# Performance work log

Hardware: AMD Instinct MI355X
Metric: run time of the kernel (lower is better)

The kernel has to match this reference:

```python
import jax, jax.numpy as jnp
import numpy as np

# Default bone connections from BoneLengthLoss.__init__
BONES = np.array([(1, 2), (1, 3), (1, 4), (2, 5), (3, 6), (11, 12), (11, 13), (12, 14),
                  (13, 14), (14, 15), (15, 16), (16, 17), (12, 18), (18, 20), (20, 22),
                  (13, 19), (19, 21), (21, 23), (16, 24), (16, 25), (24, 26), (25, 26),
                  (24, 27), (27, 29), (29, 31), (25, 28), (28, 30), (30, 32), (17, 33),
                  (33, 34), (34, 35), (35, 36)], dtype=np.int32)
J1 = jnp.asarray(BONES[:, 0])
J2 = jnp.asarray(BONES[:, 1])

BATCH = 524288
NUM_KPTS = 37


def setup_inputs() -> dict:
    key = jax.random.key(0)
    k1, k2, k3 = jax.random.split(key, 3)
    pose_3d_pred = jax.random.normal(k1, (BATCH, NUM_KPTS, 3), dtype=jnp.float32)
    pose_3d_ref = jax.random.normal(k2, (BATCH, NUM_KPTS, 3), dtype=jnp.float32)
    valid_mask = jax.random.randint(k3, (BATCH, NUM_KPTS), 0, 2).astype(jnp.bool_)
    return {"pose_3d_pred": pose_3d_pred, "pose_3d_ref": pose_3d_ref,
            "valid_mask": valid_mask}


def reference(pose_3d_pred, pose_3d_ref, valid_mask):
    # Gather both endpoints of every bone: (B, n_bones, 3)
    pred_vec = pose_3d_pred[:, J2, :] - pose_3d_pred[:, J1, :]
    ref_vec = pose_3d_ref[:, J2, :] - pose_3d_ref[:, J1, :]
    pred_len = jnp.linalg.norm(pred_vec, axis=-1)  # (B, n_bones)
    ref_len = jnp.linalg.norm(ref_vec, axis=-1)    # (B, n_bones)
    # Bone is valid iff both endpoints are valid
    bone_valid = (valid_mask[:, J1] & valid_mask[:, J2]).astype(pred_len.dtype)
    # MSE over all valid (batch, bone) entries == mean over concatenated valid lengths
    sq_err = (pred_len - ref_len) ** 2
    num = jnp.sum(sq_err * bone_valid)
    den = jnp.sum(bone_valid)
    return num / den
```

## Files before the change

### kernel.cpp

```cpp
#include <hip/hip_runtime.h>


#define NKPT   37
#define ROWF   111
#define TROWS  32
#define TF4    888
#define WF4    222
#define TMW    296
#define WMW    74
#define TMI    1184
#define WMI    296
#define BLOCK  256
#define WPB    4
#define GRID   1280

__constant__ unsigned char c_j1[32] = {1,1,1,2,3,11,11,12,13,14,15,16,12,18,20,13,19,21,16,16,24,25,24,27,29,25,28,30,17,33,34,35};
__constant__ unsigned char c_j2[32] = {2,3,4,5,6,12,13,14,14,15,16,17,18,20,22,19,21,23,24,25,26,26,27,29,31,28,30,32,33,34,35,36};

__device__ __forceinline__ void glds16(const void* g, void* l) {
    __builtin_amdgcn_global_load_lds(
        (const __attribute__((address_space(1))) void*)g,
        (__attribute__((address_space(3))) void*)l, 16, 0, 0);
}
__device__ __forceinline__ void glds4(const void* g, void* l) {
    __builtin_amdgcn_global_load_lds(
        (const __attribute__((address_space(1))) void*)g,
        (__attribute__((address_space(3))) void*)l, 4, 0, 0);
}

__global__ void init_detect(const unsigned int* __restrict__ mw,
                            unsigned int* __restrict__ ws) {
    const int tid = threadIdx.x;
    if (tid < 4) ws[tid] = 0u;
    __syncthreads();
    unsigned int local = 0;
    for (int i = tid; i < 1024; i += BLOCK) local |= mw[i] & 0xFFFFFF00u;
    if (__any(local != 0) && (tid & 63) == 0) atomicOr(&ws[2], 1u);
}

template <bool MASK_BYTES>
__device__ __forceinline__ void tile_loop(
    const float4* __restrict__ pred4, const float4* __restrict__ ref4,
    const void* __restrict__ mask, int ntiles,
    float4* s_pose, unsigned char* s_mask,
    int wave, int lane, int row, const int* j1v, const int* j2v,
    float& num, unsigned int& den)
{
    unsigned int* s_mask_w = (unsigned int*)s_mask;
    const unsigned int* __restrict__ mw = (const unsigned int*)mask;
    const int* __restrict__ mi = (const int*)mask;
    const int sb = wave * WF4;

    for (int t = blockIdx.x; t < ntiles; t += GRID) {
        const float4* pb = pred4 + (size_t)t * TF4;
        const float4* rb = ref4  + (size_t)t * TF4;

        glds16(pb + sb + lane,       &s_pose[sb]);
        glds16(pb + sb + 64 + lane,  &s_pose[sb + 64]);
        glds16(pb + sb + 128 + lane, &s_pose[sb + 128]);
        glds16(rb + sb + lane,       &s_pose[TF4 + sb]);
        glds16(rb + sb + 64 + lane,  &s_pose[TF4 + sb + 64]);
        glds16(rb + sb + 128 + lane, &s_pose[TF4 + sb + 128]);
        if (lane < WF4 - 192) {
            glds16(pb + sb + 192 + lane, &s_pose[sb + 192]);
            glds16(rb + sb + 192 + lane, &s_pose[TF4 + sb + 192]);
        }
        if (MASK_BYTES) {
            const unsigned int* mb = mw + (size_t)t * TMW + wave * WMW;
            glds4(mb + lane, &s_mask_w[wave * WMW]);
            if (lane < WMW - 64)
                glds4(mb + 64 + lane, &s_mask_w[wave * WMW + 64]);
        } else {
            const int* mb = mi + (size_t)t * TMI + wave * WMI;
#pragma unroll
            for (int j = 0; j < 5; ++j) {
                int i = lane + 64 * j;
                if (i < WMI) s_mask[wave * WMI + i] = (unsigned char)mb[i];
            }
        }
        __syncthreads();

        const float* sp = (const float*)s_pose + row * ROWF;
        const float* sr = (const float*)(s_pose + TF4) + row * ROWF;
        const unsigned char* sm = s_mask + row * NKPT;
#pragma unroll
        for (int k = 0; k < 4; ++k) {
            const int a3 = j1v[k] * 3, b3 = j2v[k] * 3;
            float dx = sp[b3] - sp[a3];
            float dy = sp[b3 + 1] - sp[a3 + 1];
            float dz = sp[b3 + 2] - sp[a3 + 2];
            float pl = sqrtf(dx * dx + dy * dy + dz * dz);
            float ex = sr[b3] - sr[a3];
            float ey = sr[b3 + 1] - sr[a3 + 1];
            float ez = sr[b3 + 2] - sr[a3 + 2];
            float rl = sqrtf(ex * ex + ey * ey + ez * ez);
            unsigned int v = (unsigned int)(sm[j1v[k]] & sm[j2v[k]]);
            float d = pl - rl;
            num += v ? d * d : 0.0f;
            den += v;
        }
        __syncthreads();
    }
}

__global__ __launch_bounds__(BLOCK, 4)
void bone_main(const float* __restrict__ pred, const float* __restrict__ ref,
               const void* __restrict__ mask, int B,
               unsigned int* __restrict__ ws, float* __restrict__ out) {
    __shared__ __align__(16) float4 s_pose[2 * TF4];
    __shared__ __align__(4) unsigned char s_mask[TMI];
    __shared__ float s_rn[WPB];
    __shared__ unsigned int s_rd[WPB];

    const int tid  = threadIdx.x;
    const int wave = tid >> 6;
    const int lane = tid & 63;
    const int row  = tid & 31;
    const int grp  = (tid >> 5) & 7;

    int j1v[4], j2v[4];
#pragma unroll
    for (int k = 0; k < 4; ++k) {
        j1v[k] = (int)c_j1[grp * 4 + k];
        j2v[k] = (int)c_j2[grp * 4 + k];
    }

    const bool mask_bytes = (ws[2] != 0);
    const int ntiles = B / TROWS;

    float num = 0.0f;
    unsigned int den = 0u;

    if (mask_bytes)
        tile_loop<true>((const float4*)pred, (const float4*)ref, mask, ntiles,
                        s_pose, s_mask, wave, lane, row, j1v, j2v, num, den);
    else
        tile_loop<false>((const float4*)pred, (const float4*)ref, mask, ntiles,
                         s_pose, s_mask, wave, lane, row, j1v, j2v, num, den);

#pragma unroll
    for (int off = 32; off > 0; off >>= 1) {
        num += __shfl_down(num, off, 64);
        den += __shfl_down(den, off, 64);
    }
    if (lane == 0) { s_rn[wave] = num; s_rd[wave] = den; }
    __syncthreads();
    if (tid == 0) {
        float n = s_rn[0] + s_rn[1] + s_rn[2] + s_rn[3];
        unsigned int d = s_rd[0] + s_rd[1] + s_rd[2] + s_rd[3];
        atomicAdd((float*)&ws[0], n);
        atomicAdd(&ws[1], d);
        __threadfence();
        unsigned int prev = atomicAdd(&ws[3], 1u);
        if (prev == (unsigned int)(gridDim.x - 1)) {
            float fn = atomicAdd((float*)&ws[0], 0.0f);
            unsigned int fd = atomicAdd(&ws[1], 0u);
            out[0] = fn / (float)fd;
        }
    }
}

extern "C" void kernel_launch(void* const* d_in, const int* in_sizes, int n_in,
                              void* d_out, int out_size, void* d_ws, size_t ws_size,
                              hipStream_t stream) {
    const float* pred = (const float*)d_in[0];
    const float* ref  = (const float*)d_in[1];
    const void*  mask = d_in[2];
    const int n_mask  = in_sizes[2];
    const int B       = n_mask / NKPT;
    unsigned int* ws  = (unsigned int*)d_ws;

    init_detect<<<1, BLOCK, 0, stream>>>((const unsigned int*)mask, ws);
    bone_main<<<GRID, BLOCK, 0, stream>>>(pred, ref, mask, B, ws, (float*)d_out);
}
```

Before: 547.0 us.

## Double tile rows, share one LDS buffer for pred then ref, compile-time bones

Result: no change. 543.0 us (-0.7%).

```diff
diff --git a/kernel.cpp b/kernel.cpp
--- a/kernel.cpp
+++ b/kernel.cpp
@@ -3,19 +3,18 @@
 
 #define NKPT   37
 #define ROWF   111
-#define TROWS  32
-#define TF4    888
-#define WF4    222
-#define TMW    296
-#define WMW    74
-#define TMI    1184
-#define WMI    296
+#define TROWS  64
+#define TF4    1776
+#define WF4    444
+#define TMB    2368
+#define TMW    592
+#define WMW    148
 #define BLOCK  256
 #define WPB    4
 #define GRID   1280
 
-__constant__ unsigned char c_j1[32] = {1,1,1,2,3,11,11,12,13,14,15,16,12,18,20,13,19,21,16,16,24,25,24,27,29,25,28,30,17,33,34,35};
-__constant__ unsigned char c_j2[32] = {2,3,4,5,6,12,13,14,14,15,16,17,18,20,22,19,21,23,24,25,26,26,27,29,31,28,30,32,33,34,35,36};
+constexpr int J1[32] = {1,1,1,2,3,11,11,12,13,14,15,16,12,18,20,13,19,21,16,16,24,25,24,27,29,25,28,30,17,33,34,35};
+constexpr int J2[32] = {2,3,4,5,6,12,13,14,14,15,16,17,18,20,22,19,21,23,24,25,26,26,27,29,31,28,30,32,33,34,35,36};
 
 __device__ __forceinline__ void glds16(const void* g, void* l) {
     __builtin_amdgcn_global_load_lds(
@@ -38,105 +37,121 @@
     if (__any(local != 0) && (tid & 63) == 0) atomicOr(&ws[2], 1u);
 }
 
-template <bool MASK_BYTES>
-__device__ __forceinline__ void tile_loop(
-    const float4* __restrict__ pred4, const float4* __restrict__ ref4,
-    const void* __restrict__ mask, int ntiles,
-    float4* s_pose, unsigned char* s_mask,
-    int wave, int lane, int row, const int* j1v, const int* j2v,
-    float& num, unsigned int& den)
-{
-    unsigned int* s_mask_w = (unsigned int*)s_mask;
-    const unsigned int* __restrict__ mw = (const unsigned int*)mask;
-    const int* __restrict__ mi = (const int*)mask;
-    const int sb = wave * WF4;
-
-    for (int t = blockIdx.x; t < ntiles; t += GRID) {
-        const float4* pb = pred4 + (size_t)t * TF4;
-        const float4* rb = ref4  + (size_t)t * TF4;
-
-        glds16(pb + sb + lane,       &s_pose[sb]);
-        glds16(pb + sb + 64 + lane,  &s_pose[sb + 64]);
-        glds16(pb + sb + 128 + lane, &s_pose[sb + 128]);
-        glds16(rb + sb + lane,       &s_pose[TF4 + sb]);
-        glds16(rb + sb + 64 + lane,  &s_pose[TF4 + sb + 64]);
-        glds16(rb + sb + 128 + lane, &s_pose[TF4 + sb + 128]);
-        if (lane < WF4 - 192) {
-            glds16(pb + sb + 192 + lane, &s_pose[sb + 192]);
-            glds16(rb + sb + 192 + lane, &s_pose[TF4 + sb + 192]);
-        }
-        if (MASK_BYTES) {
-            const unsigned int* mb = mw + (size_t)t * TMW + wave * WMW;
-            glds4(mb + lane, &s_mask_w[wave * WMW]);
-            if (lane < WMW - 64)
-                glds4(mb + 64 + lane, &s_mask_w[wave * WMW + 64]);
-        } else {
-            const int* mb = mi + (size_t)t * TMI + wave * WMI;
+template <int G>
+__device__ __forceinline__ void do_lens(const float* __restrict__ sp,
+                                        float* __restrict__ len) {
 #pragma unroll
-            for (int j = 0; j < 5; ++j) {
-                int i = lane + 64 * j;
-                if (i < WMI) s_mask[wave * WMI + i] = (unsigned char)mb[i];
-            }
-        }
-        __syncthreads();
-
-        const float* sp = (const float*)s_pose + row * ROWF;
-        const float* sr = (const float*)(s_pose + TF4) + row * ROWF;
-        const unsigned char* sm = s_mask + row * NKPT;
-#pragma unroll
-        for (int k = 0; k < 4; ++k) {
-            const int a3 = j1v[k] * 3, b3 = j2v[k] * 3;
-            float dx = sp[b3] - sp[a3];
-            float dy = sp[b3 + 1] - sp[a3 + 1];
-            float dz = sp[b3 + 2] - sp[a3 + 2];
-            float pl = sqrtf(dx * dx + dy * dy + dz * dz);
-            float ex = sr[b3] - sr[a3];
-            float ey = sr[b3 + 1] - sr[a3 + 1];
-            float ez = sr[b3 + 2] - sr[a3 + 2];
-            float rl = sqrtf(ex * ex + ey * ey + ez * ez);
-            unsigned int v = (unsigned int)(sm[j1v[k]] & sm[j2v[k]]);
-            float d = pl - rl;
-            num += v ? d * d : 0.0f;
-            den += v;
-        }
-        __syncthreads();
+    for (int k = 0; k < 8; ++k) {
+        const int a = J1[G * 8 + k] * 3, b = J2[G * 8 + k] * 3;
+        float dx = sp[b] - sp[a];
+        float dy = sp[b + 1] - sp[a + 1];
+        float dz = sp[b + 2] - sp[a + 2];
+        len[k] = __builtin_amdgcn_sqrtf(dx * dx + dy * dy + dz * dz);
     }
 }
 
-__global__ __launch_bounds__(BLOCK, 4)
+template <int G>
+__device__ __forceinline__ void do_acc(const float* __restrict__ sr,
+                                       const unsigned char* __restrict__ sm,
+                                       const float* __restrict__ plen,
+                                       float& num, unsigned int& den) {
+#pragma unroll
+    for (int k = 0; k < 8; ++k) {
+        const int a = J1[G * 8 + k], b = J2[G * 8 + k];
+        const int a3 = a * 3, b3 = b * 3;
+        float dx = sr[b3] - sr[a3];
+        float dy = sr[b3 + 1] - sr[a3 + 1];
+        float dz = sr[b3 + 2] - sr[a3 + 2];
+        float rl = __builtin_amdgcn_sqrtf(dx * dx + dy * dy + dz * dz);
+        unsigned int v = (unsigned int)(sm[a] & sm[b]);
+        float d = plen[k] - rl;
+        num += v ? d * d : 0.0f;
+        den += v;
+    }
+}
+
+__global__ __launch_bounds__(BLOCK, 5)
 void bone_main(const float* __restrict__ pred, const float* __restrict__ ref,
                const void* __restrict__ mask, int B,
                unsigned int* __restrict__ ws, float* __restrict__ out) {
-    __shared__ __align__(16) float4 s_pose[2 * TF4];
-    __shared__ __align__(4) unsigned char s_mask[TMI];
+    __shared__ __align__(16) float4 s_pose[TF4];
+    __shared__ __align__(4) unsigned char s_mask[TMB];
     __shared__ float s_rn[WPB];
     __shared__ unsigned int s_rd[WPB];
 
     const int tid  = threadIdx.x;
     const int wave = tid >> 6;
     const int lane = tid & 63;
-    const int row  = tid & 31;
-    const int grp  = (tid >> 5) & 7;
-
-    int j1v[4], j2v[4];
-#pragma unroll
-    for (int k = 0; k < 4; ++k) {
-        j1v[k] = (int)c_j1[grp * 4 + k];
-        j2v[k] = (int)c_j2[grp * 4 + k];
-    }
 
     const bool mask_bytes = (ws[2] != 0);
     const int ntiles = B / TROWS;
 
+    const float4* __restrict__ pred4 = (const float4*)pred;
+    const float4* __restrict__ ref4  = (const float4*)ref;
+    const unsigned int* __restrict__ mw = (const unsigned int*)mask;
+    const int* __restrict__ mi = (const int*)mask;
+
+    float4* s_pose_w = s_pose + wave * WF4;
+    unsigned int* s_mask_w = (unsigned int*)s_mask;
+
+    const float* sp_row = (const float*)s_pose + lane * ROWF;
+    const unsigned char* sm_row = s_mask + lane * NKPT;
+
     float num = 0.0f;
     unsigned int den = 0u;
 
-    if (mask_bytes)
-        tile_loop<true>((const float4*)pred, (const float4*)ref, mask, ntiles,
-                        s_pose, s_mask, wave, lane, row, j1v, j2v, num, den);
-    else
-        tile_loop<false>((const float4*)pred, (const float4*)ref, mask, ntiles,
-                         s_pose, s_mask, wave, lane, row, j1v, j2v, num, den);
+    for (int t = blockIdx.x; t < ntiles; t += GRID) {
+        const float4* pb = pred4 + (size_t)t * TF4 + wave * WF4;
+        const float4* rb = ref4  + (size_t)t * TF4 + wave * WF4;
+
+        glds16(pb + lane,       s_pose_w);
+        glds16(pb + 64 + lane,  s_pose_w + 64);
+        glds16(pb + 128 + lane, s_pose_w + 128);
+        glds16(pb + 192 + lane, s_pose_w + 192);
+        glds16(pb + 256 + lane, s_pose_w + 256);
+        glds16(pb + 320 + lane, s_pose_w + 320);
+        if (lane < WF4 - 384)
+            glds16(pb + 384 + lane, s_pose_w + 384);
+        if (mask_bytes) {
+            const unsigned int* mb = mw + (size_t)t * TMW + wave * WMW;
+            glds4(mb + lane,      &s_mask_w[wave * WMW]);
+            glds4(mb + 64 + lane, &s_mask_w[wave * WMW + 64]);
+            if (lane < WMW - 128)
+                glds4(mb + 128 + lane, &s_mask_w[wave * WMW + 128]);
+        } else {
+            const int* mb = mi + (size_t)t * TMB;
+            for (int i = tid; i < TMB; i += BLOCK)
+                s_mask[i] = (unsigned char)mb[i];
+        }
+        __syncthreads();
+
+        float plen[8];
+        switch (wave) {
+            case 0: do_lens<0>(sp_row, plen); break;
+            case 1: do_lens<1>(sp_row, plen); break;
+            case 2: do_lens<2>(sp_row, plen); break;
+            default: do_lens<3>(sp_row, plen); break;
+        }
+        __syncthreads();
+
+        glds16(rb + lane,       s_pose_w);
+        glds16(rb + 64 + lane,  s_pose_w + 64);
+        glds16(rb + 128 + lane, s_pose_w + 128);
+        glds16(rb + 192 + lane, s_pose_w + 192);
+        glds16(rb + 256 + lane, s_pose_w + 256);
+        glds16(rb + 320 + lane, s_pose_w + 320);
+        if (lane < WF4 - 384)
+            glds16(rb + 384 + lane, s_pose_w + 384);
+        __syncthreads();
+
+        switch (wave) {
+            case 0: do_acc<0>(sp_row, sm_row, plen, num, den); break;
+            case 1: do_acc<1>(sp_row, sm_row, plen, num, den); break;
+            case 2: do_acc<2>(sp_row, sm_row, plen, num, den); break;
+            default: do_acc<3>(sp_row, sm_row, plen, num, den); break;
+        }
+        __syncthreads();
+    }
 
 #pragma unroll
     for (int off = 32; off > 0; off >>= 1) {
```
